# Performance work log

Hardware: AMD Instinct MI355X
Metric: run time of the kernel (lower is better)

## Reference

```python
import jax, jax.numpy as jnp
import numpy as np

NH = 16
D = 1024
B, T = 4, 4096


def setup_inputs() -> dict:
    key = jax.random.key(0)
    k1, k2, k3, k4 = jax.random.split(key, 4)
    x = jax.random.normal(k1, (B, T, D), dtype=jnp.float32)
    phi = jax.random.normal(k2, (B, T), dtype=jnp.float32)
    W_attn = jax.random.normal(k3, (D, D), dtype=jnp.float32) * 0.02
    W_proj = jax.random.normal(k4, (D, D), dtype=jnp.float32) * 0.02
    gamma = jnp.ones((NH, 1), dtype=jnp.float32)
    temp = jnp.ones((NH, 1), dtype=jnp.float32)
    return {"x": x, "phi": phi, "W_attn": W_attn, "W_proj": W_proj,
            "gamma": gamma, "temp": temp}


def reference(x, phi, W_attn, W_proj, gamma, temp):
    Bb, Tt, d = x.shape
    hd = d // NH
    # c_attn (no bias), split heads: [B, nh, T, hd]
    w = (x @ W_attn.T).reshape(Bb, Tt, NH, hd).transpose(0, 2, 1, 3)
    w_sq = w * w
    denom = jnp.maximum(jnp.cumsum(w_sq, axis=-2), 1e-12)
    w_norm = w_sq / denom
    tssa_score = w_norm.sum(-1) * temp                       # [B, nh, T]
    phi_Q = phi[:, None, :]                                  # [B, 1, T]
    steps = jnp.arange(1, Tt + 1, dtype=x.dtype)
    mean_phi = jnp.cumsum(phi, axis=-1)[:, None, :] / steps  # running mean of phi
    penalty = (phi_Q - mean_phi) ** 2                        # [B, 1, T]
    score = tssa_score - gamma * penalty                     # [B, nh, T]
    alpha = jax.nn.softmax(score, axis=1)                    # softmax over HEADS (dim=1)
    dots = jnp.cumsum(w_sq * alpha[..., None], axis=-2) / (
        jnp.cumsum(alpha, axis=-1)[..., None] + 1e-8)
    attn = jnp.minimum(1.0 / (1.0 + dots), 10000.0)
    y = -w * alpha[..., None] * attn                          # [B, nh, T, hd]
    y = y.transpose(0, 2, 1, 3).reshape(Bb, Tt, d)
    y = y @ W_proj.T                                          # dropout is identity (p=0 / eval)
    return (y, alpha)
```

## Files before the change

kernel.cpp:

```cpp
#include <hip/hip_runtime.h>
#include <hip/hip_bf16.h>
#include <stdint.h>

#define NHh 16
#define Dm  1024
#define HD  64
#define Bb  4
#define Tt  4096
#define NCH 128
#define CHL 32

#define BM 256
#define BN 256
#define BK 64
#define NKT (Dm / BK)

using bf16 = __hip_bfloat16;
typedef __attribute__((ext_vector_type(8))) short short8;
typedef __attribute__((ext_vector_type(4))) float f32x4;

__device__ __forceinline__ float bf2f(bf16 v) { return __bfloat162float(v); }

__device__ __forceinline__ float b2f(unsigned short u) {
  union { unsigned int i; float f; } x; x.i = ((unsigned int)u) << 16; return x.f;
}

__device__ __forceinline__ float frcp(float x) {
  float r; asm("v_rcp_f32 %0, %1" : "=v"(r) : "v"(x)); return r;
}

__device__ __forceinline__ void gld_lds16(const void* g, void* l) {
  __builtin_amdgcn_global_load_lds(
      (const __attribute__((address_space(1))) unsigned int*)g,
      (__attribute__((address_space(3))) unsigned int*)l, 16, 0, 0);
}

__global__ void cast_f32_to_bf16(const float* __restrict__ in, bf16* __restrict__ out, int n) {
  const int stride = gridDim.x * blockDim.x;
  for (int i = blockIdx.x * blockDim.x + threadIdx.x; i * 4 < n; i += stride) {
    const float4 v = *(const float4*)(in + (size_t)i * 4);
    ushort4 o;
    o.x = __bfloat16_as_ushort(__float2bfloat16(v.x));
    o.y = __bfloat16_as_ushort(__float2bfloat16(v.y));
    o.z = __bfloat16_as_ushort(__float2bfloat16(v.z));
    o.w = __bfloat16_as_ushort(__float2bfloat16(v.w));
    *(ushort4*)(out + (size_t)i * 4) = o;
  }
}

template <bool OUT_BF16, bool WRITE_S1>
__global__ __launch_bounds__(512, 2) void gemm256(const bf16* __restrict__ A,
                                                  const bf16* __restrict__ W,
                                                  void* __restrict__ Cout,
                                                  float* __restrict__ S1,
                                                  int M, int N, int K) {
  extern __shared__ char smem[];
  const int tid  = threadIdx.x;
  const int lane = tid & 63;
  const int wave = tid >> 6;
  const int bid = blockIdx.x;
  const int swz = (bid & 7) * 32 + (bid >> 3);
  const int bn = (swz & 3) * BN;
  const int bm = (swz >> 2) * BM;
  const int wm = (wave >> 1) * 64;
  const int wn = (wave & 1) * 128;
  const int quad = lane >> 4;
  const int l16  = lane & 15;

  const int srow = wave * 8 + (lane >> 3);
  const int scol = (((lane & 7) ^ (lane >> 3)) << 3);

  const bf16* Abase = A + (size_t)(bm + srow) * K + scol;
  const bf16* Wbase = W + (size_t)(bn + srow) * K + scol;

  f32x4 acc[4][8] = {};

#define SLAB_A(buf, n) (smem + (buf) * 65536 + (n) * 8192 + wave * 1024)
#define SLAB_B(buf, n) (smem + (buf) * 65536 + 32768 + (n) * 8192 + wave * 1024)
#define STAGE_A(buf, n, k0) gld_lds16(Abase + (size_t)(n) * 64 * K + (k0), SLAB_A(buf, n))
#define STAGE_B(buf, n, k0) gld_lds16(Wbase + (size_t)(n) * 64 * K + (k0), SLAB_B(buf, n))
#define LD_FRAG(base, r, s) (*(const short8*)((base) + (size_t)(r) * 128 + ((((s) ^ ((r) & 7))) << 4)))

  STAGE_A(0, 0, 0); STAGE_A(0, 1, 0); STAGE_A(0, 2, 0); STAGE_A(0, 3, 0);
  STAGE_B(0, 0, 0); STAGE_B(0, 1, 0); STAGE_B(0, 2, 0); STAGE_B(0, 3, 0);
  asm volatile("s_waitcnt vmcnt(0)" ::: "memory");
  __builtin_amdgcn_s_barrier();
  __builtin_amdgcn_sched_barrier(0);

  short8 af[4][2], bfv[4][2];
  for (int t = 0; t < NKT; t++) {
    const int buf = t & 1;
    const char* aL = smem + buf * 65536;
    const char* bL = aL + 32768;
    const int k0n = (t + 1) * BK;
    const bool pf = (t + 1 < NKT);

    if (pf) {
      STAGE_A(buf ^ 1, 0, k0n); STAGE_A(buf ^ 1, 1, k0n);
      STAGE_A(buf ^ 1, 2, k0n); STAGE_A(buf ^ 1, 3, k0n);
      STAGE_B(buf ^ 1, 0, k0n); STAGE_B(buf ^ 1, 2, k0n);
    }
#pragma unroll
    for (int mi = 0; mi < 4; mi++) {
      const int r = wm + mi * 16 + l16;
      af[mi][0] = LD_FRAG(aL, r, quad);
      af[mi][1] = LD_FRAG(aL, r, quad + 4);
    }
#pragma unroll
    for (int nj = 0; nj < 4; nj++) {
      const int r = wn + nj * 16 + l16;
      bfv[nj][0] = LD_FRAG(bL, r, quad);
      bfv[nj][1] = LD_FRAG(bL, r, quad + 4);
    }
    __builtin_amdgcn_s_setprio(1);
#pragma unroll
    for (int mi = 0; mi < 4; mi++)
#pragma unroll
      for (int nj = 0; nj < 4; nj++) {
        acc[mi][nj] = __builtin_amdgcn_mfma_f32_16x16x32_bf16(af[mi][0], bfv[nj][0], acc[mi][nj], 0, 0, 0);
        acc[mi][nj] = __builtin_amdgcn_mfma_f32_16x16x32_bf16(af[mi][1], bfv[nj][1], acc[mi][nj], 0, 0, 0);
      }
    __builtin_amdgcn_s_setprio(0);
    if (pf) { asm volatile("s_waitcnt vmcnt(6)" ::: "memory"); }
    else    { asm volatile("s_waitcnt vmcnt(0)" ::: "memory"); }
    __builtin_amdgcn_s_barrier();
    __builtin_amdgcn_sched_barrier(0);

    if (pf) { STAGE_B(buf ^ 1, 1, k0n); STAGE_B(buf ^ 1, 3, k0n); }
#pragma unroll
    for (int nj = 0; nj < 4; nj++) {
      const int r = wn + 64 + nj * 16 + l16;
      bfv[nj][0] = LD_FRAG(bL, r, quad);
      bfv[nj][1] = LD_FRAG(bL, r, quad + 4);
    }
    __builtin_amdgcn_s_setprio(1);
#pragma unroll
    for (int mi = 0; mi < 4; mi++)
#pragma unroll
      for (int nj = 0; nj < 4; nj++) {
        acc[mi][nj + 4] = __builtin_amdgcn_mfma_f32_16x16x32_bf16(af[mi][0], bfv[nj][0], acc[mi][nj + 4], 0, 0, 0);
        acc[mi][nj + 4] = __builtin_amdgcn_mfma_f32_16x16x32_bf16(af[mi][1], bfv[nj][1], acc[mi][nj + 4], 0, 0, 0);
      }
    __builtin_amdgcn_s_setprio(0);
    asm volatile("s_waitcnt vmcnt(2)" ::: "memory");
    __builtin_amdgcn_s_barrier();
    __builtin_amdgcn_sched_barrier(0);
  }

#pragma unroll
  for (int nj = 0; nj < 8; nj++) {
    const int col = bn + wn + nj * 16 + l16;
    if constexpr (OUT_BF16) {
      float ss0 = 0.f, ss1 = 0.f;
#pragma unroll
      for (int mi = 0; mi < 4; mi++) {
        float csum = 0.f;
#pragma unroll
        for (int r = 0; r < 4; r++) {
          const int row = bm + wm + mi * 16 + quad * 4 + r;
          const bf16 hv = __float2bfloat16(acc[mi][nj][r]);
          ((bf16*)Cout)[(size_t)row * N + col] = hv;
          if constexpr (WRITE_S1) { const float fv = bf2f(hv); csum += fv * fv; }
        }
        if constexpr (WRITE_S1) { if (mi < 2) ss0 += csum; else ss1 += csum; }
      }
      if constexpr (WRITE_S1) {
        ss0 += __shfl_xor(ss0, 16, 64); ss0 += __shfl_xor(ss0, 32, 64);
        ss1 += __shfl_xor(ss1, 16, 64); ss1 += __shfl_xor(ss1, 32, 64);
        if (quad == 0) {
          const int h = col >> 6, d = col & 63;
          const int r0 = bm + wm;
          const int b  = r0 >> 12;
          const int c0 = (r0 & (Tt - 1)) >> 5;
          float* s1p = S1 + (((size_t)(b * NHh + h) * NCH) + c0) * HD + d;
          s1p[0]  = ss0;
          s1p[HD] = ss1;
        }
      }
    } else {
#pragma unroll
      for (int mi = 0; mi < 4; mi++)
#pragma unroll
        for (int r = 0; r < 4; r++) {
          const int row = bm + wm + mi * 16 + quad * 4 + r;
          ((float*)Cout)[(size_t)row * N + col] = acc[mi][nj][r];
        }
    }
  }
#undef SLAB_A
#undef SLAB_B
#undef STAGE_A
#undef STAGE_B
#undef LD_FRAG
}

__global__ __launch_bounds__(1024) void phi_penalty_kernel(const float* __restrict__ phi,
                                                           float* __restrict__ penalty) {
  const int b = blockIdx.x;
  const int tid = threadIdx.x;
  const int lane = tid & 63, wid = tid >> 6;
  __shared__ float wsum[16];
  __shared__ float carry_s;
  if (tid == 0) carry_s = 0.f;
  __syncthreads();
  for (int r = 0; r < Tt / 1024; r++) {
    const int t = r * 1024 + tid;
    const float v = phi[b * Tt + t];
    float incl = v;
#pragma unroll
    for (int off = 1; off < 64; off <<= 1) {
      float n = __shfl_up(incl, off, 64);
      if (lane >= off) incl += n;
    }
    if (lane == 63) wsum[wid] = incl;
    __syncthreads();
    float woff = carry_s;
    for (int wpre = 0; wpre < wid; wpre++) woff += wsum[wpre];
    const float csum = woff + incl;
    const float mean = csum / (float)(t + 1);
    const float dphi = v - mean;
    penalty[b * Tt + t] = dphi * dphi;
    __syncthreads();
    if (tid == 0) {
      float s = 0.f;
      for (int w = 0; w < 16; w++) s += wsum[w];
      carry_s += s;
    }
    __syncthreads();
  }
}

__global__ __launch_bounds__(64) void prefix_vec(float* __restrict__ S) {
  __shared__ float tile[NCH * HD];
  const int bh = blockIdx.x, tid = threadIdx.x;
  float* p = S + (size_t)bh * NCH * HD;
  const float4* src = (const float4*)p;
  float4* dst = (float4*)tile;
#pragma unroll 4
  for (int k = 0; k < (NCH * HD / 4) / 64; k++) dst[k * 64 + tid] = src[k * 64 + tid];
  __syncthreads();
  float run = 0.f;
  for (int c = 0; c < NCH; c++) {
    const float v = tile[c * HD + tid];
    tile[c * HD + tid] = run;
    run += v;
  }
  __syncthreads();
  float4* out = (float4*)p;
#pragma unroll 4
  for (int k = 0; k < (NCH * HD / 4) / 64; k++) out[k * 64 + tid] = dst[k * 64 + tid];
}

__global__ __launch_bounds__(64) void prefix_dots(float* __restrict__ S2, float* __restrict__ SA) {
  __shared__ float tile[NCH * HD];
  const int bh = blockIdx.x, tid = threadIdx.x;
  float* q = SA + (size_t)bh * NCH;
  const float v0 = q[tid], v1 = q[64 + tid];
  float i0 = v0;
#pragma unroll
  for (int off = 1; off < 64; off <<= 1) {
    const float n = __shfl_up(i0, off, 64);
    if (tid >= off) i0 += n;
  }
  const float tot0 = __shfl(i0, 63, 64);
  float i1 = v1;
#pragma unroll
  for (int off = 1; off < 64; off <<= 1) {
    const float n = __shfl_up(i1, off, 64);
    if (tid >= off) i1 += n;
  }
  i1 += tot0;
  q[tid] = i0 - v0;
  q[64 + tid] = i1 - v1;
  float* p = S2 + (size_t)bh * NCH * HD;
  const float4* src = (const float4*)p;
  float4* dst = (float4*)tile;
#pragma unroll 4
  for (int k = 0; k < (NCH * HD / 4) / 64; k++) dst[k * 64 + tid] = src[k * 64 + tid];
  __syncthreads();
  float run = 0.f;
  for (int c = 0; c < NCH; c++) {
    const float v = tile[c * HD + tid];
    tile[c * HD + tid] = run;
    run += v;
  }
  __syncthreads();
  float4* out = (float4*)p;
#pragma unroll 4
  for (int k = 0; k < (NCH * HD / 4) / 64; k++) out[k * 64 + tid] = dst[k * 64 + tid];
}

__global__ __launch_bounds__(256) void mid_fused(const bf16* __restrict__ w,
                                                 const float* __restrict__ S1ex,
                                                 const float* __restrict__ temp,
                                                 const float* __restrict__ gamma,
                                                 const float* __restrict__ penalty,
                                                 float* __restrict__ alpha_f,
                                                 float* __restrict__ S2,
                                                 float* __restrict__ SA) {
  const int c = blockIdx.x, b = blockIdx.y;
  const int tid = threadIdx.x, h = tid >> 4, l = tid & 15;
  __shared__ float sm_t[CHL][NHh + 1];
  __shared__ float sm_a[CHL][NHh + 1];
  __shared__ float sm_g[NHh], sm_tv[NHh];
  if (tid < NHh) { sm_g[tid] = gamma[tid]; sm_tv[tid] = temp[tid]; }
  __syncthreads();

  const bf16* wp = w + ((size_t)(b * Tt + c * CHL)) * Dm + h * HD + l * 4;
  const float4 ex = *(const float4*)&S1ex[(((size_t)(b * NHh + h) * NCH) + c) * HD + l * 4];
  float a0 = ex.x, a1 = ex.y, a2 = ex.z, a3 = ex.w;
  const float tv = sm_tv[h];
#pragma unroll 8
  for (int i = 0; i < CHL; i++) {
    const ushort4 v = *(const ushort4*)(wp + (size_t)i * Dm);
    const float f0 = b2f(v.x), f1 = b2f(v.y), f2 = b2f(v.z), f3 = b2f(v.w);
    const float s0 = f0 * f0, s1 = f1 * f1, s2 = f2 * f2, s3 = f3 * f3;
    a0 += s0; a1 += s1; a2 += s2; a3 += s3;
    float val = s0 * frcp(fmaxf(a0, 1e-12f)) + s1 * frcp(fmaxf(a1, 1e-12f))
              + s2 * frcp(fmaxf(a2, 1e-12f)) + s3 * frcp(fmaxf(a3, 1e-12f));
    val += __shfl_xor(val, 1, 64);
    val += __shfl_xor(val, 2, 64);
    val += __shfl_xor(val, 4, 64);
    val += __shfl_xor(val, 8, 64);
    if (l == 0) sm_t[i][h] = tv * val;
  }
  __syncthreads();

  if (tid < CHL) {
    const int t = tid;
    const float pen = penalty[(size_t)b * Tt + c * CHL + t];
    float sc[NHh];
    float mx = -1e30f;
#pragma unroll
    for (int hh = 0; hh < NHh; hh++) {
      sc[hh] = sm_t[t][hh] - sm_g[hh] * pen;
      mx = fmaxf(mx, sc[hh]);
    }
    float sum = 0.f;
#pragma unroll
    for (int hh = 0; hh < NHh; hh++) { const float e = __expf(sc[hh] - mx); sc[hh] = e; sum += e; }
    const float inv = 1.f / sum;
#pragma unroll
    for (int hh = 0; hh < NHh; hh++) sm_a[t][hh] = sc[hh] * inv;
  }
  __syncthreads();

#pragma unroll
  for (int k2 = 0; k2 < CHL / 16; k2++) {
    const int t = k2 * 16 + l;
    alpha_f[((size_t)(b * NHh + h)) * Tt + c * CHL + t] = sm_a[t][h];
  }

  float d0 = 0.f, d1 = 0.f, d2 = 0.f, d3 = 0.f, sa = 0.f;
#pragma unroll 8
  for (int i = 0; i < CHL; i++) {
    const float a = sm_a[i][h];
    const ushort4 v = *(const ushort4*)(wp + (size_t)i * Dm);
    const float f0 = b2f(v.x), f1 = b2f(v.y), f2 = b2f(v.z), f3 = b2f(v.w);
    d0 += f0 * f0 * a; d1 += f1 * f1 * a; d2 += f2 * f2 * a; d3 += f3 * f3 * a;
    sa += a;
  }
  float4 o; o.x = d0; o.y = d1; o.z = d2; o.w = d3;
  *(float4*)&S2[(((size_t)(b * NHh + h) * NCH) + c) * HD + l * 4] = o;
  if (l == 0) SA[(size_t)(b * NHh + h) * NCH + c] = sa;
}

__global__ __launch_bounds__(64) void y_phase3(const bf16* __restrict__ w,
                                               const float* __restrict__ alpha_f,
                                               const float* __restrict__ S2ex,
                                               const float* __restrict__ SAex,
                                               bf16* __restrict__ yprime) {
  const int g = threadIdx.x >> 4, l = threadIdx.x & 15;
  const int c = blockIdx.x * 4 + g, h = blockIdx.y, b = blockIdx.z;
  const float4 ex = *(const float4*)&S2ex[(((size_t)(b * NHh + h) * NCH) + c) * HD + l * 4];
  float a0 = ex.x, a1 = ex.y, a2 = ex.z, a3 = ex.w;
  float acca = SAex[(size_t)(b * NHh + h) * NCH + c];
  const bf16* wp = w + ((size_t)(b * Tt + c * CHL)) * Dm + h * HD + l * 4;
  const float* ap = alpha_f + (size_t)(b * NHh + h) * Tt + c * CHL;
  bf16* yp = yprime + ((size_t)(b * Tt + c * CHL)) * Dm + h * HD + l * 4;
#pragma unroll 8
  for (int i = 0; i < CHL; i++) {
    const float a = ap[i];
    const ushort4 v = *(const ushort4*)(wp + (size_t)i * Dm);
    const float f0 = b2f(v.x), f1 = b2f(v.y), f2 = b2f(v.z), f3 = b2f(v.w);
    a0 += f0 * f0 * a; a1 += f1 * f1 * a; a2 += f2 * f2 * a; a3 += f3 * f3 * a;
    acca += a;
    const float rinv = frcp(acca + 1e-8f);
    const float at0 = fminf(frcp(1.f + a0 * rinv), 10000.f);
    const float at1 = fminf(frcp(1.f + a1 * rinv), 10000.f);
    const float at2 = fminf(frcp(1.f + a2 * rinv), 10000.f);
    const float at3 = fminf(frcp(1.f + a3 * rinv), 10000.f);
    ushort4 o;
    o.x = __bfloat16_as_ushort(__float2bfloat16(-f0 * a * at0));
    o.y = __bfloat16_as_ushort(__float2bfloat16(-f1 * a * at1));
    o.z = __bfloat16_as_ushort(__float2bfloat16(-f2 * a * at2));
    o.w = __bfloat16_as_ushort(__float2bfloat16(-f3 * a * at3));
    *(ushort4*)(yp + (size_t)i * Dm) = o;
  }
}

extern "C" void kernel_launch(void* const* d_in, const int* in_sizes, int n_in,
                              void* d_out, int out_size, void* d_ws, size_t ws_size,
                              hipStream_t stream) {
  const float* x     = (const float*)d_in[0];
  const float* phi   = (const float*)d_in[1];
  const float* Wattn = (const float*)d_in[2];
  const float* Wproj = (const float*)d_in[3];
  const float* gamma = (const float*)d_in[4];
  const float* temp  = (const float*)d_in[5];

  float* y_out    = (float*)d_out;
  float* alpha_f  = y_out + (size_t)Bb * Tt * Dm;

  char* ws = (char*)d_ws;
  bf16*  x_bf   = (bf16*)ws;  ws += (size_t)Bb * Tt * Dm * 2;
  bf16*  Wa_bf  = (bf16*)ws;  ws += (size_t)Dm * Dm * 2;
  bf16*  Wp_bf  = (bf16*)ws;  ws += (size_t)Dm * Dm * 2;
  bf16*  w_bf   = (bf16*)ws;  ws += (size_t)Bb * Tt * Dm * 2;
  float* pen    = (float*)ws; ws += (size_t)Bb * Tt * 4;
  float* S1     = (float*)ws; ws += (size_t)Bb * NHh * NCH * HD * 4;
  float* S2     = (float*)ws; ws += (size_t)Bb * NHh * NCH * HD * 4;
  float* SA     = (float*)ws; ws += (size_t)Bb * NHh * NCH * 4;
  bf16*  yprime = x_bf;

  static int attr_done = 0;
  if (!attr_done) {
    hipFuncSetAttribute((const void*)gemm256<true, true>,
                        hipFuncAttributeMaxDynamicSharedMemorySize, 131072);
    hipFuncSetAttribute((const void*)gemm256<false, false>,
                        hipFuncAttributeMaxDynamicSharedMemorySize, 131072);
    attr_done = 1;
  }

  const int M = Bb * Tt, N = Dm, K = Dm;
  dim3 gg((M / BM) * (N / BN)), gb(512);
  dim3 g3(NCH / 4, NHh, Bb), b64(64);

  cast_f32_to_bf16<<<dim3(1024), dim3(256), 0, stream>>>(x, x_bf, Bb * Tt * Dm);
  cast_f32_to_bf16<<<dim3(256), dim3(256), 0, stream>>>(Wattn, Wa_bf, Dm * Dm);
  cast_f32_to_bf16<<<dim3(256), dim3(256), 0, stream>>>(Wproj, Wp_bf, Dm * Dm);

  gemm256<true, true><<<gg, gb, 131072, stream>>>(x_bf, Wa_bf, (void*)w_bf, S1, M, N, K);
  phi_penalty_kernel<<<dim3(Bb), dim3(1024), 0, stream>>>(phi, pen);
  prefix_vec<<<dim3(Bb * NHh), b64, 0, stream>>>(S1);
  mid_fused<<<dim3(NCH, Bb), dim3(256), 0, stream>>>(w_bf, S1, temp, gamma, pen,
                                                     alpha_f, S2, SA);
  prefix_dots<<<dim3(Bb * NHh), b64, 0, stream>>>(S2, SA);
  y_phase3<<<g3, b64, 0, stream>>>(w_bf, alpha_f, S2, SA, yprime);
  gemm256<false, false><<<gg, gb, 131072, stream>>>(yprime, Wp_bf, (void*)y_out, nullptr, M, N, K);
}
```

Measured before the change: 260.8 us.

## Restructure GEMM main loop into half-K slot pipeline with 2x4 wave layout

Result: slower. 269.8 us (+3.5%).

```diff
diff --git a/kernel.cpp b/kernel.cpp
--- a/kernel.cpp
+++ b/kernel.cpp
@@ -62,98 +62,125 @@
   const int swz = (bid & 7) * 32 + (bid >> 3);
   const int bn = (swz & 3) * BN;
   const int bm = (swz >> 2) * BM;
-  const int wm = (wave >> 1) * 64;
-  const int wn = (wave & 1) * 128;
+  const int wm = (wave >> 2) * 128;
+  const int wn = (wave & 3) * 64;
   const int quad = lane >> 4;
   const int l16  = lane & 15;
 
-  const int srow = wave * 8 + (lane >> 3);
-  const int scol = (((lane & 7) ^ (lane >> 3)) << 3);
-
-  const bf16* Abase = A + (size_t)(bm + srow) * K + scol;
-  const bf16* Wbase = W + (size_t)(bn + srow) * K + scol;
-
-  f32x4 acc[4][8] = {};
-
-#define SLAB_A(buf, n) (smem + (buf) * 65536 + (n) * 8192 + wave * 1024)
-#define SLAB_B(buf, n) (smem + (buf) * 65536 + 32768 + (n) * 8192 + wave * 1024)
-#define STAGE_A(buf, n, k0) gld_lds16(Abase + (size_t)(n) * 64 * K + (k0), SLAB_A(buf, n))
-#define STAGE_B(buf, n, k0) gld_lds16(Wbase + (size_t)(n) * 64 * K + (k0), SLAB_B(buf, n))
-#define LD_FRAG(base, r, s) (*(const short8*)((base) + (size_t)(r) * 128 + ((((s) ^ ((r) & 7))) << 4)))
-
-  STAGE_A(0, 0, 0); STAGE_A(0, 1, 0); STAGE_A(0, 2, 0); STAGE_A(0, 3, 0);
-  STAGE_B(0, 0, 0); STAGE_B(0, 1, 0); STAGE_B(0, 2, 0); STAGE_B(0, 3, 0);
-  asm volatile("s_waitcnt vmcnt(0)" ::: "memory");
+  const int r128 = wave * 16 + (lane >> 2);
+  const int q    = (lane & 3) ^ ((r128 >> 1) & 3);
+
+  const bf16* Asrc = A + (size_t)(bm + r128) * K + q * 8;
+  const bf16* Wsrc = W + (size_t)(bn + r128) * K + q * 8;
+
+  f32x4 acc[8][4] = {};
+
+#define SLOT(t, j) (smem + (size_t)((((t) & 1) * 4 + (j)) * 16384))
+#define STAGE(t, j) do {                                                     \
+    const bf16* s_ = ((j) & 1) ? Wsrc : Asrc;                                \
+    const int ko_ = (t) * 64 + ((j) >> 1) * 32;                              \
+    gld_lds16(s_ + ko_, SLOT(t, j) + wave * 1024);                           \
+    gld_lds16(s_ + (size_t)128 * K + ko_, SLOT(t, j) + 8192 + wave * 1024);  \
+  } while (0)
+#define LD_FRAG(sb, r, c) (*(const short8*)((sb) + (size_t)(r) * 64 + ((((c) ^ (((r) >> 1) & 3))) << 4)))
+
+  STAGE(0, 0); STAGE(0, 1); STAGE(0, 2); STAGE(0, 3);
+  STAGE(1, 0); STAGE(1, 1);
+  asm volatile("s_waitcnt vmcnt(4)" ::: "memory");
   __builtin_amdgcn_s_barrier();
   __builtin_amdgcn_sched_barrier(0);
 
-  short8 af[4][2], bfv[4][2];
+  short8 Af[4], Bk[4];
   for (int t = 0; t < NKT; t++) {
-    const int buf = t & 1;
-    const char* aL = smem + buf * 65536;
-    const char* bL = aL + 32768;
-    const int k0n = (t + 1) * BK;
-    const bool pf = (t + 1 < NKT);
-
-    if (pf) {
-      STAGE_A(buf ^ 1, 0, k0n); STAGE_A(buf ^ 1, 1, k0n);
-      STAGE_A(buf ^ 1, 2, k0n); STAGE_A(buf ^ 1, 3, k0n);
-      STAGE_B(buf ^ 1, 0, k0n); STAGE_B(buf ^ 1, 2, k0n);
-    }
-#pragma unroll
-    for (int mi = 0; mi < 4; mi++) {
-      const int r = wm + mi * 16 + l16;
-      af[mi][0] = LD_FRAG(aL, r, quad);
-      af[mi][1] = LD_FRAG(aL, r, quad + 4);
-    }
-#pragma unroll
-    for (int nj = 0; nj < 4; nj++) {
-      const int r = wn + nj * 16 + l16;
-      bfv[nj][0] = LD_FRAG(bL, r, quad);
-      bfv[nj][1] = LD_FRAG(bL, r, quad + 4);
-    }
+    const char* A0 = SLOT(t, 0);
+    const char* B0 = SLOT(t, 1);
+    const char* A1 = SLOT(t, 2);
+    const char* B1 = SLOT(t, 3);
+    const bool pf1 = (t + 1 < NKT);
+    const bool pf2 = (t + 2 < NKT);
+
+#pragma unroll
+    for (int nj = 0; nj < 4; nj++) Bk[nj] = LD_FRAG(B0, wn + nj * 16 + l16, quad);
+#pragma unroll
+    for (int mi = 0; mi < 4; mi++) Af[mi] = LD_FRAG(A0, wm + mi * 16 + l16, quad);
+    if (pf1) STAGE(t + 1, 2);
+    __builtin_amdgcn_sched_barrier(0);
+    __builtin_amdgcn_s_barrier();
+    asm volatile("s_waitcnt lgkmcnt(0)" ::: "memory");
+    __builtin_amdgcn_sched_barrier(0);
     __builtin_amdgcn_s_setprio(1);
 #pragma unroll
     for (int mi = 0; mi < 4; mi++)
 #pragma unroll
-      for (int nj = 0; nj < 4; nj++) {
-        acc[mi][nj] = __builtin_amdgcn_mfma_f32_16x16x32_bf16(af[mi][0], bfv[nj][0], acc[mi][nj], 0, 0, 0);
-        acc[mi][nj] = __builtin_amdgcn_mfma_f32_16x16x32_bf16(af[mi][1], bfv[nj][1], acc[mi][nj], 0, 0, 0);
-      }
+      for (int nj = 0; nj < 4; nj++)
+        acc[mi][nj] = __builtin_amdgcn_mfma_f32_16x16x32_bf16(Af[mi], Bk[nj], acc[mi][nj], 0, 0, 0);
     __builtin_amdgcn_s_setprio(0);
-    if (pf) { asm volatile("s_waitcnt vmcnt(6)" ::: "memory"); }
-    else    { asm volatile("s_waitcnt vmcnt(0)" ::: "memory"); }
-    __builtin_amdgcn_s_barrier();
-    __builtin_amdgcn_sched_barrier(0);
-
-    if (pf) { STAGE_B(buf ^ 1, 1, k0n); STAGE_B(buf ^ 1, 3, k0n); }
-#pragma unroll
-    for (int nj = 0; nj < 4; nj++) {
-      const int r = wn + 64 + nj * 16 + l16;
-      bfv[nj][0] = LD_FRAG(bL, r, quad);
-      bfv[nj][1] = LD_FRAG(bL, r, quad + 4);
-    }
+    __builtin_amdgcn_sched_barrier(0);
+    __builtin_amdgcn_s_barrier();
+
+#pragma unroll
+    for (int mi = 0; mi < 4; mi++) Af[mi] = LD_FRAG(A0, wm + 64 + mi * 16 + l16, quad);
+    if (pf1) STAGE(t + 1, 3);
+    __builtin_amdgcn_sched_barrier(0);
+    __builtin_amdgcn_s_barrier();
+    asm volatile("s_waitcnt lgkmcnt(0)" ::: "memory");
+    __builtin_amdgcn_sched_barrier(0);
     __builtin_amdgcn_s_setprio(1);
 #pragma unroll
     for (int mi = 0; mi < 4; mi++)
 #pragma unroll
-      for (int nj = 0; nj < 4; nj++) {
-        acc[mi][nj + 4] = __builtin_amdgcn_mfma_f32_16x16x32_bf16(af[mi][0], bfv[nj][0], acc[mi][nj + 4], 0, 0, 0);
-        acc[mi][nj + 4] = __builtin_amdgcn_mfma_f32_16x16x32_bf16(af[mi][1], bfv[nj][1], acc[mi][nj + 4], 0, 0, 0);
-      }
+      for (int nj = 0; nj < 4; nj++)
+        acc[mi + 4][nj] = __builtin_amdgcn_mfma_f32_16x16x32_bf16(Af[mi], Bk[nj], acc[mi + 4][nj], 0, 0, 0);
     __builtin_amdgcn_s_setprio(0);
-    asm volatile("s_waitcnt vmcnt(2)" ::: "memory");
-    __builtin_amdgcn_s_barrier();
-    __builtin_amdgcn_sched_barrier(0);
-  }
-
-#pragma unroll
-  for (int nj = 0; nj < 8; nj++) {
+    __builtin_amdgcn_sched_barrier(0);
+    __builtin_amdgcn_s_barrier();
+
+#pragma unroll
+    for (int nj = 0; nj < 4; nj++) Bk[nj] = LD_FRAG(B1, wn + nj * 16 + l16, quad);
+#pragma unroll
+    for (int mi = 0; mi < 4; mi++) Af[mi] = LD_FRAG(A1, wm + mi * 16 + l16, quad);
+    if (pf2) STAGE(t + 2, 0);
+    __builtin_amdgcn_sched_barrier(0);
+    __builtin_amdgcn_s_barrier();
+    asm volatile("s_waitcnt lgkmcnt(0)" ::: "memory");
+    __builtin_amdgcn_sched_barrier(0);
+    __builtin_amdgcn_s_setprio(1);
+#pragma unroll
+    for (int mi = 0; mi < 4; mi++)
+#pragma unroll
+      for (int nj = 0; nj < 4; nj++)
+        acc[mi][nj] = __builtin_amdgcn_mfma_f32_16x16x32_bf16(Af[mi], Bk[nj], acc[mi][nj], 0, 0, 0);
+    __builtin_amdgcn_s_setprio(0);
+    __builtin_amdgcn_sched_barrier(0);
+    __builtin_amdgcn_s_barrier();
+
+#pragma unroll
+    for (int mi = 0; mi < 4; mi++) Af[mi] = LD_FRAG(A1, wm + 64 + mi * 16 + l16, quad);
+    if (pf2) STAGE(t + 2, 1);
+    __builtin_amdgcn_sched_barrier(0);
+    __builtin_amdgcn_s_barrier();
+    asm volatile("s_waitcnt lgkmcnt(0)" ::: "memory");
+    __builtin_amdgcn_sched_barrier(0);
+    __builtin_amdgcn_s_setprio(1);
+#pragma unroll
+    for (int mi = 0; mi < 4; mi++)
+#pragma unroll
+      for (int nj = 0; nj < 4; nj++)
+        acc[mi + 4][nj] = __builtin_amdgcn_mfma_f32_16x16x32_bf16(Af[mi], Bk[nj], acc[mi + 4][nj], 0, 0, 0);
+    __builtin_amdgcn_s_setprio(0);
+    if (t < NKT - 2) { asm volatile("s_waitcnt vmcnt(4)" ::: "memory"); }
+    else             { asm volatile("s_waitcnt vmcnt(0)" ::: "memory"); }
+    __builtin_amdgcn_sched_barrier(0);
+    __builtin_amdgcn_s_barrier();
+  }
+
+#pragma unroll
+  for (int nj = 0; nj < 4; nj++) {
     const int col = bn + wn + nj * 16 + l16;
     if constexpr (OUT_BF16) {
-      float ss0 = 0.f, ss1 = 0.f;
-#pragma unroll
-      for (int mi = 0; mi < 4; mi++) {
+      float ss0 = 0.f, ss1 = 0.f, ss2 = 0.f, ss3 = 0.f;
+#pragma unroll
+      for (int mi = 0; mi < 8; mi++) {
         float csum = 0.f;
 #pragma unroll
         for (int r = 0; r < 4; r++) {
@@ -162,24 +189,33 @@
           ((bf16*)Cout)[(size_t)row * N + col] = hv;
           if constexpr (WRITE_S1) { const float fv = bf2f(hv); csum += fv * fv; }
         }
-        if constexpr (WRITE_S1) { if (mi < 2) ss0 += csum; else ss1 += csum; }
+        if constexpr (WRITE_S1) {
+          if (mi < 2) ss0 += csum;
+          else if (mi < 4) ss1 += csum;
+          else if (mi < 6) ss2 += csum;
+          else ss3 += csum;
+        }
       }
       if constexpr (WRITE_S1) {
         ss0 += __shfl_xor(ss0, 16, 64); ss0 += __shfl_xor(ss0, 32, 64);
         ss1 += __shfl_xor(ss1, 16, 64); ss1 += __shfl_xor(ss1, 32, 64);
+        ss2 += __shfl_xor(ss2, 16, 64); ss2 += __shfl_xor(ss2, 32, 64);
+        ss3 += __shfl_xor(ss3, 16, 64); ss3 += __shfl_xor(ss3, 32, 64);
         if (quad == 0) {
           const int h = col >> 6, d = col & 63;
           const int r0 = bm + wm;
           const int b  = r0 >> 12;
           const int c0 = (r0 & (Tt - 1)) >> 5;
           float* s1p = S1 + (((size_t)(b * NHh + h) * NCH) + c0) * HD + d;
-          s1p[0]  = ss0;
-          s1p[HD] = ss1;
+          s1p[0]      = ss0;
+          s1p[HD]     = ss1;
+          s1p[2 * HD] = ss2;
+          s1p[3 * HD] = ss3;
         }
       }
     } else {
 #pragma unroll
-      for (int mi = 0; mi < 4; mi++)
+      for (int mi = 0; mi < 8; mi++)
 #pragma unroll
         for (int r = 0; r < 4; r++) {
           const int row = bm + wm + mi * 16 + quad * 4 + r;
@@ -187,10 +223,8 @@
         }
     }
   }
-#undef SLAB_A
-#undef SLAB_B
-#undef STAGE_A
-#undef STAGE_B
+#undef SLOT
+#undef STAGE
 #undef LD_FRAG
 }
 
```

## Fuse casts and phi penalty into one prep kernel; fold chunk prefix scans into consumers

Applied to the files above, without the earlier changes.

Result: slower. 268.3 us (+2.9%).

```diff
diff --git a/kernel.cpp b/kernel.cpp
--- a/kernel.cpp
+++ b/kernel.cpp
@@ -33,19 +33,6 @@
   __builtin_amdgcn_global_load_lds(
       (const __attribute__((address_space(1))) unsigned int*)g,
       (__attribute__((address_space(3))) unsigned int*)l, 16, 0, 0);
-}
-
-__global__ void cast_f32_to_bf16(const float* __restrict__ in, bf16* __restrict__ out, int n) {
-  const int stride = gridDim.x * blockDim.x;
-  for (int i = blockIdx.x * blockDim.x + threadIdx.x; i * 4 < n; i += stride) {
-    const float4 v = *(const float4*)(in + (size_t)i * 4);
-    ushort4 o;
-    o.x = __bfloat16_as_ushort(__float2bfloat16(v.x));
-    o.y = __bfloat16_as_ushort(__float2bfloat16(v.y));
-    o.z = __bfloat16_as_ushort(__float2bfloat16(v.z));
-    o.w = __bfloat16_as_ushort(__float2bfloat16(v.w));
-    *(ushort4*)(out + (size_t)i * 4) = o;
-  }
 }
 
 template <bool OUT_BF16, bool WRITE_S1>
@@ -194,104 +181,66 @@
 #undef LD_FRAG
 }
 
-__global__ __launch_bounds__(1024) void phi_penalty_kernel(const float* __restrict__ phi,
-                                                           float* __restrict__ penalty) {
-  const int b = blockIdx.x;
-  const int tid = threadIdx.x;
-  const int lane = tid & 63, wid = tid >> 6;
-  __shared__ float wsum[16];
-  __shared__ float carry_s;
-  if (tid == 0) carry_s = 0.f;
-  __syncthreads();
-  for (int r = 0; r < Tt / 1024; r++) {
-    const int t = r * 1024 + tid;
-    const float v = phi[b * Tt + t];
-    float incl = v;
-#pragma unroll
-    for (int off = 1; off < 64; off <<= 1) {
-      float n = __shfl_up(incl, off, 64);
-      if (lane >= off) incl += n;
-    }
-    if (lane == 63) wsum[wid] = incl;
+__global__ __launch_bounds__(256) void prep(const float* __restrict__ x,
+                                            const float* __restrict__ Wa,
+                                            const float* __restrict__ Wp,
+                                            const float* __restrict__ phi,
+                                            bf16* __restrict__ x_bf,
+                                            bf16* __restrict__ Wa_bf,
+                                            bf16* __restrict__ Wp_bf,
+                                            float* __restrict__ penalty) {
+  const int bid = blockIdx.x;
+  if (bid < 1536) {
+    const float* in;
+    bf16* out;
+    int n, nblk, b0;
+    if (bid < 1024)      { in = x;  out = x_bf;  n = Bb * Tt * Dm; nblk = 1024; b0 = 0; }
+    else if (bid < 1280) { in = Wa; out = Wa_bf; n = Dm * Dm;      nblk = 256;  b0 = 1024; }
+    else                 { in = Wp; out = Wp_bf; n = Dm * Dm;      nblk = 256;  b0 = 1280; }
+    const int stride = nblk * 256;
+    for (int i = (bid - b0) * 256 + threadIdx.x; i * 4 < n; i += stride) {
+      const float4 v = *(const float4*)(in + (size_t)i * 4);
+      ushort4 o;
+      o.x = __bfloat16_as_ushort(__float2bfloat16(v.x));
+      o.y = __bfloat16_as_ushort(__float2bfloat16(v.y));
+      o.z = __bfloat16_as_ushort(__float2bfloat16(v.z));
+      o.w = __bfloat16_as_ushort(__float2bfloat16(v.w));
+      *(ushort4*)(out + (size_t)i * 4) = o;
+    }
+  } else {
+    const int b = bid - 1536;
+    const int tid = threadIdx.x;
+    const int lane = tid & 63, wid = tid >> 6;
+    __shared__ float wsum[4];
+    __shared__ float carry_s;
+    if (tid == 0) carry_s = 0.f;
     __syncthreads();
-    float woff = carry_s;
-    for (int wpre = 0; wpre < wid; wpre++) woff += wsum[wpre];
-    const float csum = woff + incl;
-    const float mean = csum / (float)(t + 1);
-    const float dphi = v - mean;
-    penalty[b * Tt + t] = dphi * dphi;
-    __syncthreads();
-    if (tid == 0) {
-      float s = 0.f;
-      for (int w = 0; w < 16; w++) s += wsum[w];
-      carry_s += s;
-    }
-    __syncthreads();
-  }
-}
-
-__global__ __launch_bounds__(64) void prefix_vec(float* __restrict__ S) {
-  __shared__ float tile[NCH * HD];
-  const int bh = blockIdx.x, tid = threadIdx.x;
-  float* p = S + (size_t)bh * NCH * HD;
-  const float4* src = (const float4*)p;
-  float4* dst = (float4*)tile;
-#pragma unroll 4
-  for (int k = 0; k < (NCH * HD / 4) / 64; k++) dst[k * 64 + tid] = src[k * 64 + tid];
-  __syncthreads();
-  float run = 0.f;
-  for (int c = 0; c < NCH; c++) {
-    const float v = tile[c * HD + tid];
-    tile[c * HD + tid] = run;
-    run += v;
-  }
-  __syncthreads();
-  float4* out = (float4*)p;
-#pragma unroll 4
-  for (int k = 0; k < (NCH * HD / 4) / 64; k++) out[k * 64 + tid] = dst[k * 64 + tid];
-}
-
-__global__ __launch_bounds__(64) void prefix_dots(float* __restrict__ S2, float* __restrict__ SA) {
-  __shared__ float tile[NCH * HD];
-  const int bh = blockIdx.x, tid = threadIdx.x;
-  float* q = SA + (size_t)bh * NCH;
-  const float v0 = q[tid], v1 = q[64 + tid];
-  float i0 = v0;
-#pragma unroll
-  for (int off = 1; off < 64; off <<= 1) {
-    const float n = __shfl_up(i0, off, 64);
-    if (tid >= off) i0 += n;
-  }
-  const float tot0 = __shfl(i0, 63, 64);
-  float i1 = v1;
-#pragma unroll
-  for (int off = 1; off < 64; off <<= 1) {
-    const float n = __shfl_up(i1, off, 64);
-    if (tid >= off) i1 += n;
-  }
-  i1 += tot0;
-  q[tid] = i0 - v0;
-  q[64 + tid] = i1 - v1;
-  float* p = S2 + (size_t)bh * NCH * HD;
-  const float4* src = (const float4*)p;
-  float4* dst = (float4*)tile;
-#pragma unroll 4
-  for (int k = 0; k < (NCH * HD / 4) / 64; k++) dst[k * 64 + tid] = src[k * 64 + tid];
-  __syncthreads();
-  float run = 0.f;
-  for (int c = 0; c < NCH; c++) {
-    const float v = tile[c * HD + tid];
-    tile[c * HD + tid] = run;
-    run += v;
-  }
-  __syncthreads();
-  float4* out = (float4*)p;
-#pragma unroll 4
-  for (int k = 0; k < (NCH * HD / 4) / 64; k++) out[k * 64 + tid] = dst[k * 64 + tid];
+    for (int r = 0; r < Tt / 256; r++) {
+      const int t = r * 256 + tid;
+      const float v = phi[b * Tt + t];
+      float incl = v;
+#pragma unroll
+      for (int off = 1; off < 64; off <<= 1) {
+        float nn = __shfl_up(incl, off, 64);
+        if (lane >= off) incl += nn;
+      }
+      if (lane == 63) wsum[wid] = incl;
+      __syncthreads();
+      float woff = carry_s;
+      for (int wpre = 0; wpre < wid; wpre++) woff += wsum[wpre];
+      const float csum = woff + incl;
+      const float mean = csum / (float)(t + 1);
+      const float dphi = v - mean;
+      penalty[b * Tt + t] = dphi * dphi;
+      __syncthreads();
+      if (tid == 0) carry_s += wsum[0] + wsum[1] + wsum[2] + wsum[3];
+      __syncthreads();
+    }
+  }
 }
 
 __global__ __launch_bounds__(256) void mid_fused(const bf16* __restrict__ w,
-                                                 const float* __restrict__ S1ex,
+                                                 const float* __restrict__ S1,
                                                  const float* __restrict__ temp,
                                                  const float* __restrict__ gamma,
                                                  const float* __restrict__ penalty,
@@ -304,11 +253,22 @@
   __shared__ float sm_a[CHL][NHh + 1];
   __shared__ float sm_g[NHh], sm_tv[NHh];
   if (tid < NHh) { sm_g[tid] = gamma[tid]; sm_tv[tid] = temp[tid]; }
+
+  const float4* p4 = (const float4*)(S1 + (((size_t)(b * NHh + h) * NCH)) * HD + l * 4);
+  float bx = 0.f, by = 0.f, bz = 0.f, bw = 0.f;
+  float cx = 0.f, cy = 0.f, cz = 0.f, cw = 0.f;
+  int cc = 0;
+  for (; cc + 2 <= c; cc += 2) {
+    const float4 v0 = p4[(size_t)cc * 16];
+    const float4 v1 = p4[(size_t)(cc + 1) * 16];
+    bx += v0.x; by += v0.y; bz += v0.z; bw += v0.w;
+    cx += v1.x; cy += v1.y; cz += v1.z; cw += v1.w;
+  }
+  if (cc < c) { const float4 v0 = p4[(size_t)cc * 16]; bx += v0.x; by += v0.y; bz += v0.z; bw += v0.w; }
+  float a0 = bx + cx, a1 = by + cy, a2 = bz + cz, a3 = bw + cw;
   __syncthreads();
 
   const bf16* wp = w + ((size_t)(b * Tt + c * CHL)) * Dm + h * HD + l * 4;
-  const float4 ex = *(const float4*)&S1ex[(((size_t)(b * NHh + h) * NCH) + c) * HD + l * 4];
-  float a0 = ex.x, a1 = ex.y, a2 = ex.z, a3 = ex.w;
   const float tv = sm_tv[h];
 #pragma unroll 8
   for (int i = 0; i < CHL; i++) {
@@ -367,14 +327,33 @@
 
 __global__ __launch_bounds__(64) void y_phase3(const bf16* __restrict__ w,
                                                const float* __restrict__ alpha_f,
-                                               const float* __restrict__ S2ex,
-                                               const float* __restrict__ SAex,
+                                               const float* __restrict__ S2,
+                                               const float* __restrict__ SA,
                                                bf16* __restrict__ yprime) {
   const int g = threadIdx.x >> 4, l = threadIdx.x & 15;
   const int c = blockIdx.x * 4 + g, h = blockIdx.y, b = blockIdx.z;
-  const float4 ex = *(const float4*)&S2ex[(((size_t)(b * NHh + h) * NCH) + c) * HD + l * 4];
-  float a0 = ex.x, a1 = ex.y, a2 = ex.z, a3 = ex.w;
-  float acca = SAex[(size_t)(b * NHh + h) * NCH + c];
+
+  const float4* p4 = (const float4*)(S2 + (((size_t)(b * NHh + h) * NCH)) * HD + l * 4);
+  const float* sap = SA + (size_t)(b * NHh + h) * NCH;
+  float bx = 0.f, by = 0.f, bz = 0.f, bw = 0.f;
+  float cx = 0.f, cy = 0.f, cz = 0.f, cw = 0.f;
+  float sa0 = 0.f, sa1 = 0.f;
+  int cc = 0;
+  for (; cc + 2 <= c; cc += 2) {
+    const float4 v0 = p4[(size_t)cc * 16];
+    const float4 v1 = p4[(size_t)(cc + 1) * 16];
+    bx += v0.x; by += v0.y; bz += v0.z; bw += v0.w;
+    cx += v1.x; cy += v1.y; cz += v1.z; cw += v1.w;
+    sa0 += sap[cc]; sa1 += sap[cc + 1];
+  }
+  if (cc < c) {
+    const float4 v0 = p4[(size_t)cc * 16];
+    bx += v0.x; by += v0.y; bz += v0.z; bw += v0.w;
+    sa0 += sap[cc];
+  }
+  float a0 = bx + cx, a1 = by + cy, a2 = bz + cz, a3 = bw + cw;
+  float acca = sa0 + sa1;
+
   const bf16* wp = w + ((size_t)(b * Tt + c * CHL)) * Dm + h * HD + l * 4;
   const float* ap = alpha_f + (size_t)(b * NHh + h) * Tt + c * CHL;
   bf16* yp = yprime + ((size_t)(b * Tt + c * CHL)) * Dm + h * HD + l * 4;
@@ -434,18 +413,11 @@
 
   const int M = Bb * Tt, N = Dm, K = Dm;
   dim3 gg((M / BM) * (N / BN)), gb(512);
-  dim3 g3(NCH / 4, NHh, Bb), b64(64);
-
-  cast_f32_to_bf16<<<dim3(1024), dim3(256), 0, stream>>>(x, x_bf, Bb * Tt * Dm);
-  cast_f32_to_bf16<<<dim3(256), dim3(256), 0, stream>>>(Wattn, Wa_bf, Dm * Dm);
-  cast_f32_to_bf16<<<dim3(256), dim3(256), 0, stream>>>(Wproj, Wp_bf, Dm * Dm);
-
+
+  prep<<<dim3(1540), dim3(256), 0, stream>>>(x, Wattn, Wproj, phi, x_bf, Wa_bf, Wp_bf, pen);
   gemm256<true, true><<<gg, gb, 131072, stream>>>(x_bf, Wa_bf, (void*)w_bf, S1, M, N, K);
-  phi_penalty_kernel<<<dim3(Bb), dim3(1024), 0, stream>>>(phi, pen);
-  prefix_vec<<<dim3(Bb * NHh), b64, 0, stream>>>(S1);
   mid_fused<<<dim3(NCH, Bb), dim3(256), 0, stream>>>(w_bf, S1, temp, gamma, pen,
                                                      alpha_f, S2, SA);
-  prefix_dots<<<dim3(Bb * NHh), b64, 0, stream>>>(S2, SA);
-  y_phase3<<<g3, b64, 0, stream>>>(w_bf, alpha_f, S2, SA, yprime);
+  y_phase3<<<dim3(NCH / 4, NHh, Bb), dim3(64), 0, stream>>>(w_bf, alpha_f, S2, SA, yprime);
   gemm256<false, false><<<gg, gb, 131072, stream>>>(yprime, Wp_bf, (void*)y_out, nullptr, M, N, K);
 }
```
